# Performance work log

Hardware: AMD Instinct MI355X
Metric: run time of the kernel (lower is better)

## Reference

```python
import jax, jax.numpy as jnp
import numpy as np

B, C, H, W = 8, 768, 32, 32
NH = 12
HD = C // NH
HID = 4 * C
EPS = 1e-5


def _layer_norm(x, g, b):
    mu = jnp.mean(x, axis=-1, keepdims=True)
    var = jnp.mean(jnp.square(x - mu), axis=-1, keepdims=True)
    return (x - mu) * jax.lax.rsqrt(var + EPS) * g + b


def setup_inputs() -> dict:
    key = jax.random.key(0)
    ks = jax.random.split(key, 12)
    s = 0.02
    return {
        "x": jax.random.normal(ks[0], (B, C, H, W), jnp.float32),
        "conv_w": jax.random.normal(ks[1], (C, 1, 3, 3), jnp.float32) * s,  # depthwise OIHW
        "conv_b": jnp.zeros((C,), jnp.float32),
        "ln1_g": jnp.ones((C,), jnp.float32),
        "ln1_b": jnp.zeros((C,), jnp.float32),
        "qkv_w": jax.random.normal(ks[2], (3 * C, C), jnp.float32) * s,  # no bias (qkv_bias=False)
        "proj_w": jax.random.normal(ks[3], (C, C), jnp.float32) * s,
        "proj_b": jnp.zeros((C,), jnp.float32),
        "ln2_g": jnp.ones((C,), jnp.float32),
        "ln2_b": jnp.zeros((C,), jnp.float32),
        "fc1_w": jax.random.normal(ks[4], (HID, C), jnp.float32) * s,
        "fc1_b": jnp.zeros((HID,), jnp.float32),
        "fc2_w": jax.random.normal(ks[5], (C, HID), jnp.float32) * s,
        "fc2_b": jnp.zeros((C,), jnp.float32),
    }


def reference(x, conv_w, conv_b, ln1_g, ln1_b, qkv_w, proj_w, proj_b,
              ln2_g, ln2_b, fc1_w, fc1_b, fc2_w, fc2_b):
    # depthwise 3x3 conv positional embedding, residual
    pe = jax.lax.conv_general_dilated(
        x, conv_w, window_strides=(1, 1), padding=((1, 1), (1, 1)),
        dimension_numbers=("NCHW", "OIHW", "NCHW"), feature_group_count=C)
    x = x + pe + conv_b[None, :, None, None]

    b, c, h, w = x.shape
    t = x.reshape(b, c, h * w).transpose(0, 2, 1)  # [B, N, C]

    # attention
    hn = _layer_norm(t, ln1_g, ln1_b)
    qkv = hn @ qkv_w.T  # [B, N, 3C]
    qkv = qkv.reshape(b, h * w, 3, NH, HD).transpose(2, 0, 3, 1, 4)  # [3, B, nh, N, hd]
    q, k, v = qkv[0], qkv[1], qkv[2]
    scale = HD ** -0.5
    attn = jax.nn.softmax(jnp.einsum("bhnd,bhmd->bhnm", q, k) * scale, axis=-1)
    o = jnp.einsum("bhnm,bhmd->bhnd", attn, v).transpose(0, 2, 1, 3).reshape(b, h * w, c)
    t = t + (o @ proj_w.T + proj_b)

    # MLP
    hn = _layer_norm(t, ln2_g, ln2_b)
    hid = jax.nn.gelu(hn @ fc1_w.T + fc1_b, approximate=False)
    t = t + (hid @ fc2_w.T + fc2_b)

    return t.transpose(0, 2, 1).reshape(b, c, h, w)
```

## Files before the change

kernel.cpp:

```cpp
#include <hip/hip_runtime.h>
#include <math.h>


typedef __bf16 bf16;
typedef __attribute__((ext_vector_type(8))) __bf16 bf16x8;
typedef __attribute__((ext_vector_type(4))) __bf16 bf16x4;
typedef __attribute__((ext_vector_type(4))) float f32x4;

#define B_   8
#define C_   768
#define N_   1024
#define NH_  12
#define HD_  64
#define HID_ 3072
#define NTOK   (B_ * N_)
#define NHEADS (B_ * NH_)
#define FA_C   0.1803368801111601f

__device__ __forceinline__ void gload_lds16(const void* g, void* l) {
  __builtin_amdgcn_global_load_lds(
      (__attribute__((address_space(1))) void*)(void*)g,
      (__attribute__((address_space(3))) void*)l, 16, 0, 0);
}

__device__ __forceinline__ float gelu1(float x) {
  float u = 0.7978845608028654f * x * (1.0f + 0.044715f * x * x);
  float e = __builtin_amdgcn_exp2f(u * 2.885390081777927f);
  float th = 1.0f - 2.0f * __builtin_amdgcn_rcpf(e + 1.0f);
  return 0.5f * x * (1.0f + th);
}

#define PIPE_SYNC(N)                                              \
  do {                                                            \
    asm volatile("s_waitcnt vmcnt(" #N ") lgkmcnt(0)" ::: "memory"); \
    __builtin_amdgcn_sched_barrier(0);                            \
    __builtin_amdgcn_s_barrier();                                 \
    __builtin_amdgcn_sched_barrier(0);                            \
    asm volatile("" ::: "memory");                                \
  } while (0)

__global__ __launch_bounds__(512) void gemm_fc1(
    const bf16* __restrict__ A, const bf16* __restrict__ Bw,
    const float* __restrict__ bias, bf16* __restrict__ outp,
    int K, int lda, int ldb, int ntiles, int mtpx, int ldo) {
  __shared__ __align__(16) char smem[114688];
  const int tid = threadIdx.x;
  const int wave = tid >> 6, lane = tid & 63;
  const int wr = wave & 1, wc = wave >> 1;
  const int lr = lane & 15, kq = lane >> 4;

  const int bid = blockIdx.x;
  const int g = bid & 7, s = bid >> 3;
  const int ms = s / ntiles;
  const int m0 = (g * mtpx + ms) * 256;
  const int n0 = (s - ms * ntiles) * 192;

  f32x4 acc[8][3];
#pragma unroll
  for (int i = 0; i < 8; ++i)
#pragma unroll
    for (int j = 0; j < 3; ++j) acc[i][j] = (f32x4){0.f, 0.f, 0.f, 0.f};

  const bf16* pa[4];
  const bf16* pb[3];
  int da[4], db[3];
#pragma unroll
  for (int c = 0; c < 4; ++c) {
    const int sidx = c * 512 + tid;
    const int r = sidx >> 3, seg = (sidx & 7) ^ (r & 7);
    pa[c] = A + (size_t)(m0 + r) * lda + seg * 8;
    da[c] = sidx * 16;
  }
#pragma unroll
  for (int c = 0; c < 3; ++c) {
    const int sidx = c * 512 + tid;
    const int r = sidx >> 3, seg = (sidx & 7) ^ (r & 7);
    pb[c] = Bw + (size_t)(n0 + r) * ldb + seg * 8;
    db[c] = 32768 + sidx * 16;
  }

  const int NT = K >> 6;

  gload_lds16(pb[0], smem + db[0]);
  gload_lds16(pb[1], smem + db[1]);
  gload_lds16(pb[2], smem + db[2]);
  gload_lds16(pa[0], smem + da[0]);
  gload_lds16(pa[1], smem + da[1]);
  gload_lds16(pa[2], smem + da[2]);
  gload_lds16(pa[3], smem + da[3]);
#pragma unroll
  for (int c = 0; c < 4; ++c) pa[c] += 64;
#pragma unroll
  for (int c = 0; c < 3; ++c) pb[c] += 64;

  for (int t = 0; t < NT - 1; ++t) {
    const char* rb = smem + (t & 1) * 57344;
    char* wb = smem + ((t & 1) ^ 1) * 57344;
    bf16x8 af[4], bf0[3], bf1[3];

    PIPE_SYNC(1);
#pragma unroll
    for (int i = 0; i < 4; ++i) {
      const int r = wr * 128 + i * 16 + lr;
      af[i] = *(const bf16x8*)(rb + (r * 8 + (kq ^ (r & 7))) * 16);
    }
#pragma unroll
    for (int j = 0; j < 3; ++j) {
      const int r = wc * 48 + j * 16 + lr;
      bf0[j] = *(const bf16x8*)(rb + 32768 + (r * 8 + (kq ^ (r & 7))) * 16);
    }
    gload_lds16(pb[0], wb + db[0]); pb[0] += 64;
    gload_lds16(pb[1], wb + db[1]); pb[1] += 64;
    __builtin_amdgcn_s_setprio(1);
#pragma unroll
    for (int i = 0; i < 4; ++i)
#pragma unroll
      for (int j = 0; j < 3; ++j)
        acc[i][j] = __builtin_amdgcn_mfma_f32_16x16x32_bf16(bf0[j], af[i],
                                                            acc[i][j], 0, 0, 0);
    __builtin_amdgcn_s_setprio(0);

    PIPE_SYNC(2);
#pragma unroll
    for (int i = 0; i < 4; ++i) {
      const int r = wr * 128 + 64 + i * 16 + lr;
      af[i] = *(const bf16x8*)(rb + (r * 8 + (kq ^ (r & 7))) * 16);
    }
    gload_lds16(pb[2], wb + db[2]); pb[2] += 64;
    gload_lds16(pa[0], wb + da[0]); pa[0] += 64;
    __builtin_amdgcn_s_setprio(1);
#pragma unroll
    for (int i = 0; i < 4; ++i)
#pragma unroll
      for (int j = 0; j < 3; ++j)
        acc[4 + i][j] = __builtin_amdgcn_mfma_f32_16x16x32_bf16(
            bf0[j], af[i], acc[4 + i][j], 0, 0, 0);
    __builtin_amdgcn_s_setprio(0);

    PIPE_SYNC(4);
#pragma unroll
    for (int i = 0; i < 4; ++i) {
      const int r = wr * 128 + i * 16 + lr;
      af[i] = *(const bf16x8*)(rb + (r * 8 + ((4 + kq) ^ (r & 7))) * 16);
    }
#pragma unroll
    for (int j = 0; j < 3; ++j) {
      const int r = wc * 48 + j * 16 + lr;
      bf1[j] = *(const bf16x8*)(rb + 32768 + (r * 8 + ((4 + kq) ^ (r & 7))) * 16);
    }
    gload_lds16(pa[1], wb + da[1]); pa[1] += 64;
    gload_lds16(pa[2], wb + da[2]); pa[2] += 64;
    __builtin_amdgcn_s_setprio(1);
#pragma unroll
    for (int i = 0; i < 4; ++i)
#pragma unroll
      for (int j = 0; j < 3; ++j)
        acc[i][j] = __builtin_amdgcn_mfma_f32_16x16x32_bf16(bf1[j], af[i],
                                                            acc[i][j], 0, 0, 0);
    __builtin_amdgcn_s_setprio(0);

    PIPE_SYNC(6);
#pragma unroll
    for (int i = 0; i < 4; ++i) {
      const int r = wr * 128 + 64 + i * 16 + lr;
      af[i] = *(const bf16x8*)(rb + (r * 8 + ((4 + kq) ^ (r & 7))) * 16);
    }
    gload_lds16(pa[3], wb + da[3]); pa[3] += 64;
    __builtin_amdgcn_s_setprio(1);
#pragma unroll
    for (int i = 0; i < 4; ++i)
#pragma unroll
      for (int j = 0; j < 3; ++j)
        acc[4 + i][j] = __builtin_amdgcn_mfma_f32_16x16x32_bf16(
            bf1[j], af[i], acc[4 + i][j], 0, 0, 0);
    __builtin_amdgcn_s_setprio(0);
  }

  {
    const char* rb = smem + ((NT - 1) & 1) * 57344;
    bf16x8 af[4], bf0[3], bf1[3];
    PIPE_SYNC(0);
#pragma unroll
    for (int j = 0; j < 3; ++j) {
      const int r = wc * 48 + j * 16 + lr;
      bf0[j] = *(const bf16x8*)(rb + 32768 + (r * 8 + (kq ^ (r & 7))) * 16);
      bf1[j] = *(const bf16x8*)(rb + 32768 + (r * 8 + ((4 + kq) ^ (r & 7))) * 16);
    }
    __builtin_amdgcn_s_setprio(1);
#pragma unroll
    for (int half = 0; half < 2; ++half) {
#pragma unroll
      for (int i = 0; i < 4; ++i) {
        const int r = wr * 128 + half * 64 + i * 16 + lr;
        af[i] = *(const bf16x8*)(rb + (r * 8 + (kq ^ (r & 7))) * 16);
      }
#pragma unroll
      for (int i = 0; i < 4; ++i)
#pragma unroll
        for (int j = 0; j < 3; ++j)
          acc[half * 4 + i][j] = __builtin_amdgcn_mfma_f32_16x16x32_bf16(
              bf0[j], af[i], acc[half * 4 + i][j], 0, 0, 0);
#pragma unroll
      for (int i = 0; i < 4; ++i) {
        const int r = wr * 128 + half * 64 + i * 16 + lr;
        af[i] = *(const bf16x8*)(rb + (r * 8 + ((4 + kq) ^ (r & 7))) * 16);
      }
#pragma unroll
      for (int i = 0; i < 4; ++i)
#pragma unroll
        for (int j = 0; j < 3; ++j)
          acc[half * 4 + i][j] = __builtin_amdgcn_mfma_f32_16x16x32_bf16(
              bf1[j], af[i], acc[half * 4 + i][j], 0, 0, 0);
    }
    __builtin_amdgcn_s_setprio(0);
  }

#pragma unroll
  for (int j = 0; j < 3; ++j) {
    const int n = n0 + wc * 48 + j * 16 + kq * 4;
    const f32x4 bv = *(const f32x4*)(bias + n);
#pragma unroll
    for (int i = 0; i < 8; ++i) {
      const int m = m0 + wr * 128 + i * 16 + lr;
      const f32x4 v = acc[i][j];
      bf16x4 pk = {(bf16)gelu1(v[0] + bv[0]), (bf16)gelu1(v[1] + bv[1]),
                   (bf16)gelu1(v[2] + bv[2]), (bf16)gelu1(v[3] + bv[3])};
      *(bf16x4*)(outp + (size_t)m * ldo + n) = pk;
    }
  }
}

template <int BN, int EPI, bool REMAP>
__global__ __launch_bounds__(256) void gemm_bt(
    const bf16* __restrict__ A, const bf16* __restrict__ B, int K, int lda,
    int ldb, int ntiles, bf16* __restrict__ o0, bf16* __restrict__ o1,
    bf16* __restrict__ o2, float* __restrict__ resid,
    const float* __restrict__ bias, float* __restrict__ outp) {
  constexpr int JJ = BN / 32;
  constexpr int BCH = BN / 32;
  constexpr int STAGE_B = (128 + BN) * 64 * 2;
  constexpr int EXTRA_B = (EPI == 5) ? 64 * 132 * 4 : (EPI == 0 ? 128 * 256 : 0);
  constexpr int SMEM_B = STAGE_B > EXTRA_B ? STAGE_B : EXTRA_B;
  __shared__ __align__(16) char smemraw[SMEM_B];
  bf16* As = (bf16*)smemraw;
  bf16* Bs = As + 128 * 64;

  const int tid = threadIdx.x;
  const int wave = tid >> 6, lane = tid & 63;
  const int wm = wave & 1, wn = wave >> 1;
  const int lr = lane & 15, kq = lane >> 4;
  const int sw = lr & 7;

  int m0, n0;
  if constexpr (REMAP) {
    const int bid = blockIdx.x;
    const int g = bid & 7, s = bid >> 3;
    const int ms = s / ntiles;
    m0 = (g * 8 + ms) * 128;
    n0 = (s - ms * ntiles) * BN;
  } else {
    m0 = blockIdx.y * 128;
    n0 = blockIdx.x * BN;
  }

  f32x4 acc[4][JJ];
#pragma unroll
  for (int i = 0; i < 4; i++)
#pragma unroll
    for (int j = 0; j < JJ; j++) acc[i][j] = (f32x4){0.f, 0.f, 0.f, 0.f};

  const bf16* ap[4];
  const bf16* bp[BCH];
  {
    const bf16* Arow = A + (size_t)m0 * lda;
    const bf16* Brow = B + (size_t)n0 * ldb;
#pragma unroll
    for (int it = 0; it < 4; ++it) {
      int s = it * 256 + tid;
      int r = s >> 3, seg = (s & 7) ^ (r & 7);
      ap[it] = Arow + (size_t)r * lda + seg * 8;
    }
#pragma unroll
    for (int it = 0; it < BCH; ++it) {
      int s = it * 256 + tid;
      int r = s >> 3, seg = (s & 7) ^ (r & 7);
      bp[it] = Brow + (size_t)r * ldb + seg * 8;
    }
  }

  for (int k0 = 0; k0 < K; k0 += 64) {
#pragma unroll
    for (int it = 0; it < 4; ++it) {
      gload_lds16(ap[it], (char*)As + (it * 256 + tid) * 16);
      ap[it] += 64;
    }
#pragma unroll
    for (int it = 0; it < BCH; ++it) {
      gload_lds16(bp[it], (char*)Bs + (it * 256 + tid) * 16);
      bp[it] += 64;
    }
    __syncthreads();

#pragma unroll
    for (int h = 0; h < 2; ++h) {
      bf16x8 af[4], bfr[JJ];
      const int c = h * 4 + kq;
#pragma unroll
      for (int i = 0; i < 4; i++) {
        int row = wm * 64 + i * 16 + lr;
        af[i] = *(const bf16x8*)((char*)As + (row * 8 + (c ^ sw)) * 16);
      }
#pragma unroll
      for (int j = 0; j < JJ; j++) {
        int row = wn * (BN / 2) + j * 16 + lr;
        bfr[j] = *(const bf16x8*)((char*)Bs + (row * 8 + (c ^ sw)) * 16);
      }
#pragma unroll
      for (int i = 0; i < 4; i++)
#pragma unroll
        for (int j = 0; j < JJ; j++)
          acc[i][j] = __builtin_amdgcn_mfma_f32_16x16x32_bf16(bfr[j], af[i],
                                                              acc[i][j], 0, 0, 0);
    }
    __syncthreads();
  }

  if constexpr (EPI == 0) {
    const int b = m0 >> 10, tok0 = m0 & (N_ - 1);
    if (n0 < 2 * C_) {
      const int s = n0 >= C_ ? 1 : 0;
      bf16* dst = s ? o1 : o0;
#pragma unroll
      for (int i = 0; i < 4; i++) {
        const int m = m0 + wm * 64 + i * 16 + lr;
#pragma unroll
        for (int j = 0; j < JJ; j++) {
          const int rem = n0 - s * C_ + wn * (BN / 2) + j * 16 + kq * 4;
          const int h = rem >> 6, d = rem & 63;
          const f32x4 v = acc[i][j];
          bf16x4 pk = {(bf16)v[0], (bf16)v[1], (bf16)v[2], (bf16)v[3]};
          size_t head = (size_t)b * NH_ + h;
          *(bf16x4*)(dst + (head * N_ + (m & (N_ - 1))) * HD_ + d) = pk;
        }
      }
    } else {
      bf16* tile = (bf16*)smemraw;
#pragma unroll
      for (int i = 0; i < 4; i++) {
        const int ml = wm * 64 + i * 16 + lr;
        const int mc = ml >> 3, mo = ml & 7;
#pragma unroll
        for (int j = 0; j < JJ; j++) {
          const f32x4 v = acc[i][j];
#pragma unroll
          for (int r = 0; r < 4; r++) {
            const int nl = wn * (BN / 2) + j * 16 + kq * 4 + r;
            *(bf16*)((char*)tile + nl * 256 + ((mc ^ (nl & 15)) * 16) + mo * 2) =
                (bf16)v[r];
          }
        }
      }
      __syncthreads();
      const int nl = tid >> 1, mh = (tid & 1) * 64;
      const int vb = n0 - 2 * C_ + nl;
      const size_t head = (size_t)b * NH_ + (vb >> 6);
      bf16* dst = o2 + (head * HD_ + (vb & 63)) * N_ + tok0 + mh;
#pragma unroll
      for (int c8 = 0; c8 < 8; ++c8) {
        const int c = (mh >> 3) + c8;
        bf16x8 val = *(const bf16x8*)((char*)tile + nl * 256 +
                                      ((c ^ (nl & 15)) * 16));
        *(bf16x8*)(dst + c8 * 8) = val;
      }
    }
  } else if constexpr (EPI == 3) {
#pragma unroll
    for (int j = 0; j < JJ; j++) {
      const int n = n0 + wn * (BN / 2) + j * 16 + kq * 4;
      const f32x4 bv = *(const f32x4*)(bias + n);
#pragma unroll
      for (int i = 0; i < 4; i++) {
        const int m = m0 + wm * 64 + i * 16 + lr;
        float* rp = resid + (size_t)m * C_ + n;
        f32x4 old = *(const f32x4*)rp;
        const f32x4 v = acc[i][j];
        f32x4 nw = {old[0] + v[0] + bv[0], old[1] + v[1] + bv[1],
                    old[2] + v[2] + bv[2], old[3] + v[3] + bv[3]};
        *(f32x4*)rp = nw;
      }
    }
  } else if constexpr (EPI == 5) {
    float* tile = (float*)smemraw;
    const int b = m0 >> 10, tok0 = m0 & (N_ - 1);
#pragma unroll
    for (int j = 0; j < JJ; j++) {
      const int nl0 = wn * (BN / 2) + j * 16 + kq * 4;
      const int n = n0 + nl0;
      const f32x4 bv = *(const f32x4*)(bias + n);
#pragma unroll
      for (int i = 0; i < 4; i++) {
        const int ml = wm * 64 + i * 16 + lr;
        const float* rp = resid + (size_t)(m0 + ml) * C_ + n;
        f32x4 old = *(const f32x4*)rp;
        const f32x4 v = acc[i][j];
#pragma unroll
        for (int r = 0; r < 4; r++)
          tile[(nl0 + r) * 132 + ml] = old[r] + v[r] + bv[r];
      }
    }
    __syncthreads();
    const int nl = tid & 63, mc = tid >> 6;
    float* dst = outp + ((size_t)(b * C_ + n0 + nl)) * N_ + tok0 + mc * 32;
    const float* src = tile + nl * 132 + mc * 32;
#pragma unroll
    for (int q = 0; q < 8; ++q)
      *(f32x4*)(dst + q * 4) = *(const f32x4*)(src + q * 4);
  }
}

__global__ __launch_bounds__(256, 3) void flash_attn(
    const bf16* __restrict__ Qb, const bf16* __restrict__ Kb,
    const bf16* __restrict__ Vt, bf16* __restrict__ attn) {
  __shared__ __align__(16) bf16 ksm[2][64 * 64];
  __shared__ __align__(16) bf16 vsm[2][64 * 64];
  __shared__ __align__(16) bf16 psm[4][32 * 64];

  const int tid = threadIdx.x, wave = tid >> 6, lane = tid & 63;
  const int lr = lane & 15, kq = lane >> 4;
  const int head = blockIdx.y;
  const int b = head / NH_, hh = head - b * NH_;
  const int q0 = blockIdx.x * 128;
  const bf16* Qh = Qb + (size_t)head * (N_ * HD_);
  const bf16* Kh = Kb + (size_t)head * (N_ * HD_);
  const bf16* Vh = Vt + (size_t)head * (HD_ * N_);
  char* pw = (char*)&psm[wave][0];

  bf16x8 qf[2][2];
#pragma unroll
  for (int j = 0; j < 2; ++j)
#pragma unroll
    for (int kh = 0; kh < 2; ++kh)
      qf[j][kh] = *(const bf16x8*)(Qh +
                                   (size_t)(q0 + wave * 32 + j * 16 + lr) * HD_ +
                                   kh * 32 + kq * 8);

  f32x4 o[4][2];
#pragma unroll
  for (int i = 0; i < 4; i++)
#pragma unroll
    for (int j = 0; j < 2; j++) o[i][j] = (f32x4){0.f, 0.f, 0.f, 0.f};
  float mprev[2] = {-1e30f, -1e30f}, lacc[2] = {0.f, 0.f};

  auto stage = [&](int t, int bi) {
#pragma unroll
    for (int it = 0; it < 2; ++it) {
      int s = it * 256 + tid;
      int r = s >> 3, seg = (s & 7) ^ (r & 7);
      gload_lds16(Kh + (size_t)(t * 64 + r) * HD_ + seg * 8,
                  (char*)ksm[bi] + (it * 256 + wave * 64) * 16);
    }
#pragma unroll
    for (int it = 0; it < 2; ++it) {
      int s = it * 256 + tid;
      int r = s >> 3, seg = (s & 7) ^ (r & 7);
      gload_lds16(Vh + (size_t)r * N_ + t * 64 + seg * 8,
                  (char*)vsm[bi] + (it * 256 + wave * 64) * 16);
    }
  };

  stage(0, 0);

  for (int t = 0; t < 16; ++t) {
    const int bi = t & 1;
    __syncthreads();
    if (t < 15) stage(t + 1, bi ^ 1);

    f32x4 sacc[4][2];
#pragma unroll
    for (int i = 0; i < 4; ++i) {
#pragma unroll
      for (int j = 0; j < 2; ++j) sacc[i][j] = (f32x4){0.f, 0.f, 0.f, 0.f};
      int row = i * 16 + lr;
      bf16x8 kf0 = *(const bf16x8*)((char*)ksm[bi] + row * 128 +
                                    ((kq ^ (row & 7)) * 16));
      bf16x8 kf1 = *(const bf16x8*)((char*)ksm[bi] + row * 128 +
                                    (((4 + kq) ^ (row & 7)) * 16));
#pragma unroll
      for (int j = 0; j < 2; ++j) {
        sacc[i][j] = __builtin_amdgcn_mfma_f32_16x16x32_bf16(kf0, qf[j][0],
                                                             sacc[i][j], 0, 0, 0);
        sacc[i][j] = __builtin_amdgcn_mfma_f32_16x16x32_bf16(kf1, qf[j][1],
                                                             sacc[i][j], 0, 0, 0);
      }
    }

#pragma unroll
    for (int j = 0; j < 2; ++j) {
      float mx = -1e30f;
#pragma unroll
      for (int i = 0; i < 4; ++i)
#pragma unroll
        for (int r = 0; r < 4; ++r) mx = fmaxf(mx, sacc[i][j][r]);
      mx = fmaxf(mx, __shfl_xor(mx, 16));
      mx = fmaxf(mx, __shfl_xor(mx, 32));
      float mnew = fmaxf(mprev[j], mx);
      float alpha = __builtin_amdgcn_exp2f((mprev[j] - mnew) * FA_C);
      mprev[j] = mnew;
      float rs = 0.f;
      const int prow = j * 16 + lr;
#pragma unroll
      for (int i = 0; i < 4; ++i) {
        float p0 = __builtin_amdgcn_exp2f((sacc[i][j][0] - mnew) * FA_C);
        float p1 = __builtin_amdgcn_exp2f((sacc[i][j][1] - mnew) * FA_C);
        float p2 = __builtin_amdgcn_exp2f((sacc[i][j][2] - mnew) * FA_C);
        float p3 = __builtin_amdgcn_exp2f((sacc[i][j][3] - mnew) * FA_C);
        rs += (p0 + p1) + (p2 + p3);
        bf16x4 pk = {(bf16)p0, (bf16)p1, (bf16)p2, (bf16)p3};
        int c = i * 2 + (kq >> 1);
        *(bf16x4*)(pw + prow * 128 + ((c ^ (prow & 7)) * 16) + (kq & 1) * 8) = pk;
      }
      rs += __shfl_xor(rs, 16);
      rs += __shfl_xor(rs, 32);
      lacc[j] = lacc[j] * alpha + rs;
#pragma unroll
      for (int i = 0; i < 4; ++i) {
        o[i][j][0] *= alpha; o[i][j][1] *= alpha;
        o[i][j][2] *= alpha; o[i][j][3] *= alpha;
      }
    }

#pragma unroll
    for (int k0c = 0; k0c < 2; ++k0c) {
      bf16x8 pf[2];
#pragma unroll
      for (int j = 0; j < 2; ++j) {
        int prow = j * 16 + lr, c = k0c * 4 + kq;
        pf[j] = *(const bf16x8*)(pw + prow * 128 + ((c ^ (prow & 7)) * 16));
      }
#pragma unroll
      for (int i = 0; i < 4; ++i) {
        int d = i * 16 + lr, c = k0c * 4 + kq;
        bf16x8 vf = *(const bf16x8*)((char*)vsm[bi] + d * 128 +
                                     ((c ^ (d & 7)) * 16));
#pragma unroll
        for (int j = 0; j < 2; ++j)
          o[i][j] = __builtin_amdgcn_mfma_f32_16x16x32_bf16(vf, pf[j], o[i][j],
                                                            0, 0, 0);
      }
    }
  }

#pragma unroll
  for (int j = 0; j < 2; ++j) {
    float inv = 1.0f / lacc[j];
    int tok = q0 + wave * 32 + j * 16 + lr;
    bf16* op = attn + ((size_t)(b * N_ + tok)) * C_ + hh * HD_;
#pragma unroll
    for (int i = 0; i < 4; ++i) {
      bf16x4 pk = {(bf16)(o[i][j][0] * inv), (bf16)(o[i][j][1] * inv),
                   (bf16)(o[i][j][2] * inv), (bf16)(o[i][j][3] * inv)};
      *(bf16x4*)(op + i * 16 + kq * 4) = pk;
    }
  }
}

__global__ __launch_bounds__(256) void cast_all(
    const float* __restrict__ a, int na, const float* __restrict__ b, int nb,
    const float* __restrict__ c, int nc, const float* __restrict__ d,
    bf16* __restrict__ dst) {
  int i = (blockIdx.x * 256 + threadIdx.x) * 4;
  const float* src;
  int off;
  if (i < na) { src = a; off = i; }
  else if (i < na + nb) { src = b; off = i - na; }
  else if (i < na + nb + nc) { src = c; off = i - na - nb; }
  else { src = d; off = i - na - nb - nc; }
  float4 v = *(const float4*)(src + off);
  bf16x4 o = {(bf16)v.x, (bf16)v.y, (bf16)v.z, (bf16)v.w};
  *(bf16x4*)(dst + i) = o;
}

__global__ __launch_bounds__(256) void conv_pe_t(const float* __restrict__ x,
                                                 const float* __restrict__ cw,
                                                 const float* __restrict__ cb,
                                                 float* __restrict__ t0) {
  __shared__ float tile[32][33];
  const int h = blockIdx.x, ct = blockIdx.y, b = blockIdx.z;
  const int tid = threadIdx.x;
  const int w = tid & 31, cs = tid >> 5;
#pragma unroll
  for (int cc = cs; cc < 32; cc += 8) {
    int c = ct * 32 + cc;
    const float* xp = x + ((size_t)(b * C_ + c)) * 1024;
    const float* wp = cw + c * 9;
    float s = cb[c] + xp[h * 32 + w];
#pragma unroll
    for (int ky = 0; ky < 3; ++ky) {
      int hy = h + ky - 1;
      if ((unsigned)hy < 32u) {
#pragma unroll
        for (int kx = 0; kx < 3; ++kx) {
          int wx = w + kx - 1;
          if ((unsigned)wx < 32u) s += xp[hy * 32 + wx] * wp[ky * 3 + kx];
        }
      }
    }
    tile[cc][w] = s;
  }
  __syncthreads();
  const int cc = tid & 31;
#pragma unroll
  for (int wc = tid >> 5; wc < 32; wc += 8)
    t0[((size_t)(b * N_) + h * 32 + wc) * C_ + ct * 32 + cc] = tile[cc][wc];
}

__global__ __launch_bounds__(256) void ln_bf16(const float* __restrict__ t,
                                               const float* __restrict__ g,
                                               const float* __restrict__ be,
                                               bf16* __restrict__ out) {
  int row = blockIdx.x, tid = threadIdx.x;
  const float* p = t + (size_t)row * C_;
  float v0 = p[tid], v1 = p[tid + 256], v2 = p[tid + 512];
  __shared__ float rs[256], rq[256];
  rs[tid] = v0 + v1 + v2;
  rq[tid] = v0 * v0 + v1 * v1 + v2 * v2;
  __syncthreads();
  for (int off = 128; off; off >>= 1) {
    if (tid < off) {
      rs[tid] += rs[tid + off];
      rq[tid] += rq[tid + off];
    }
    __syncthreads();
  }
  float mu = rs[0] * (1.f / C_);
  float var = rq[0] * (1.f / C_) - mu * mu;
  float rstd = rsqrtf(var + 1e-5f);
  bf16* q = out + (size_t)row * C_;
  q[tid] = (bf16)((v0 - mu) * rstd * g[tid] + be[tid]);
  q[tid + 256] = (bf16)((v1 - mu) * rstd * g[tid + 256] + be[tid + 256]);
  q[tid + 512] = (bf16)((v2 - mu) * rstd * g[tid + 512] + be[tid + 512]);
}

extern "C" void kernel_launch(void* const* d_in, const int* in_sizes, int n_in,
                              void* d_out, int out_size, void* d_ws,
                              size_t ws_size, hipStream_t stream) {
  (void)in_sizes; (void)n_in; (void)out_size; (void)ws_size;
  const float* x      = (const float*)d_in[0];
  const float* conv_w = (const float*)d_in[1];
  const float* conv_b = (const float*)d_in[2];
  const float* ln1_g  = (const float*)d_in[3];
  const float* ln1_b  = (const float*)d_in[4];
  const float* qkv_w  = (const float*)d_in[5];
  const float* proj_w = (const float*)d_in[6];
  const float* proj_b = (const float*)d_in[7];
  const float* ln2_g  = (const float*)d_in[8];
  const float* ln2_b  = (const float*)d_in[9];
  const float* fc1_w  = (const float*)d_in[10];
  const float* fc1_b  = (const float*)d_in[11];
  const float* fc2_w  = (const float*)d_in[12];
  const float* fc2_b  = (const float*)d_in[13];
  float* out = (float*)d_out;

  char* w = (char*)d_ws;
  auto carve = [&](size_t bytes) {
    char* p = w;
    w += (bytes + 255) & ~(size_t)255;
    return p;
  };
  bf16* hid   = (bf16*)carve((size_t)NTOK * HID_ * 2);
  float* t0   = (float*)carve((size_t)NTOK * C_ * 4);
  bf16* lnout = (bf16*)carve((size_t)NTOK * C_ * 2);
  bf16* wq    = (bf16*)carve((size_t)3 * C_ * C_ * 2);
  bf16* wp    = (bf16*)carve((size_t)C_ * C_ * 2);
  bf16* w1    = (bf16*)carve((size_t)HID_ * C_ * 2);
  bf16* w2    = (bf16*)carve((size_t)C_ * HID_ * 2);
  bf16* Qb    = (bf16*)carve((size_t)NHEADS * N_ * HD_ * 2);
  bf16* Kb    = (bf16*)carve((size_t)NHEADS * N_ * HD_ * 2);
  bf16* Vt    = (bf16*)carve((size_t)NHEADS * HD_ * N_ * 2);
  bf16* attn  = (bf16*)carve((size_t)NTOK * C_ * 2);

  const int na = 3 * C_ * C_, nb = C_ * C_, nc = HID_ * C_, nd = C_ * HID_;
  cast_all<<<(na + nb + nc + nd) / 1024, 256, 0, stream>>>(
      qkv_w, na, proj_w, nb, fc1_w, nc, fc2_w, wq);

  conv_pe_t<<<dim3(32, C_ / 32, B_), 256, 0, stream>>>(x, conv_w, conv_b, t0);

  ln_bf16<<<NTOK, 256, 0, stream>>>(t0, ln1_g, ln1_b, lnout);
  gemm_bt<128, 0, true><<<1152, 256, 0, stream>>>(
      lnout, wq, 768, 768, 768, 18, Qb, Kb, Vt, nullptr, nullptr, nullptr);

  flash_attn<<<dim3(N_ / 128, NHEADS), 256, 0, stream>>>(Qb, Kb, Vt, attn);

  gemm_bt<64, 3, true><<<768, 256, 0, stream>>>(
      attn, wp, 768, 768, 768, 12, nullptr, nullptr, nullptr, t0, proj_b,
      nullptr);
  ln_bf16<<<NTOK, 256, 0, stream>>>(t0, ln2_g, ln2_b, lnout);
  gemm_fc1<<<512, 512, 0, stream>>>(lnout, w1, fc1_b, hid, 768, 768, 768,
                                    16, 4, HID_);
  gemm_bt<64, 5, true><<<768, 256, 0, stream>>>(
      hid, w2, 3072, 3072, 3072, 12, nullptr, nullptr, nullptr, t0, fc2_b,
      out);
}
```

Measured before the change: 385.7 us.

## Add dedicated 512-thread triple-buffered FC2 GEMM with larger N tile

Replaces the generic gemm_bt<64,5> FC2 kernel with a dedicated 512-thread kernel. It uses 128x192 tiles, a three-stage global-to-LDS pipeline with direct LDS loads, and a sliced transposed residual epilogue. The larger tiles are meant to raise data reuse and cut redundant A loads over K=3072, and the deeper pipeline hides memory latency. The launch drops to 256 blocks, which may leave some CUs underused, and the large LDS footprint limits occupancy to one block per CU.

New measurement: 395.2 us. +2.5%, slower.

```diff
diff --git a/kernel.cpp b/kernel.cpp
--- a/kernel.cpp
+++ b/kernel.cpp
@@ -39,6 +39,176 @@
     asm volatile("" ::: "memory");                                \
   } while (0)
 
+__global__ __launch_bounds__(512) void gemm_fc2(
+    const bf16* __restrict__ A, const bf16* __restrict__ Bw,
+    const float* __restrict__ bias, const float* __restrict__ resid,
+    float* __restrict__ outp, int K, int lda, int ldb) {
+  __shared__ __align__(16) char smem[122880];
+  const int tid = threadIdx.x;
+  const int wave = tid >> 6, lane = tid & 63;
+  const int wr = wave & 1, wc = wave >> 1;
+  const int lr = lane & 15, kq = lane >> 4;
+
+  const int bid = blockIdx.x;
+  const int g = bid & 7, s = bid >> 3;
+  const int ms = s >> 2;
+  const int m0 = (g * 8 + ms) * 128;
+  const int n0 = (s & 3) * 192;
+
+  f32x4 acc[4][3];
+#pragma unroll
+  for (int i = 0; i < 4; ++i)
+#pragma unroll
+    for (int j = 0; j < 3; ++j) acc[i][j] = (f32x4){0.f, 0.f, 0.f, 0.f};
+
+  const bf16* pa[2];
+  const bf16* pb[3];
+  int da[2], db[3];
+#pragma unroll
+  for (int c = 0; c < 2; ++c) {
+    const int sidx = c * 512 + tid;
+    const int r = sidx >> 3, seg = (sidx & 7) ^ (r & 7);
+    pa[c] = A + (size_t)(m0 + r) * lda + seg * 8;
+    da[c] = sidx * 16;
+  }
+#pragma unroll
+  for (int c = 0; c < 3; ++c) {
+    const int sidx = c * 512 + tid;
+    const int r = sidx >> 3, seg = (sidx & 7) ^ (r & 7);
+    pb[c] = Bw + (size_t)(n0 + r) * ldb + seg * 8;
+    db[c] = 16384 + sidx * 16;
+  }
+
+  const int NT = K >> 6;
+
+#pragma unroll
+  for (int tt = 0; tt < 2; ++tt) {
+    char* wb = smem + tt * 40960;
+    gload_lds16(pb[0], wb + db[0]);
+    gload_lds16(pb[1], wb + db[1]);
+    gload_lds16(pb[2], wb + db[2]);
+    gload_lds16(pa[0], wb + da[0]);
+    gload_lds16(pa[1], wb + da[1]);
+    pb[0] += 64; pb[1] += 64; pb[2] += 64; pa[0] += 64; pa[1] += 64;
+  }
+
+  int cur = 0;
+  for (int t = 0; t < NT - 1; ++t) {
+    const char* rb = smem + cur * 40960;
+    PIPE_SYNC(5);
+    if (t < NT - 2) {
+      int wi = cur + 2; if (wi >= 3) wi -= 3;
+      char* wb = smem + wi * 40960;
+      gload_lds16(pb[0], wb + db[0]); pb[0] += 64;
+      gload_lds16(pb[1], wb + db[1]); pb[1] += 64;
+      gload_lds16(pb[2], wb + db[2]); pb[2] += 64;
+      gload_lds16(pa[0], wb + da[0]); pa[0] += 64;
+      gload_lds16(pa[1], wb + da[1]); pa[1] += 64;
+    }
+    bf16x8 af[4], bf[3];
+#pragma unroll
+    for (int i = 0; i < 4; ++i) {
+      const int r = wr * 64 + i * 16 + lr;
+      af[i] = *(const bf16x8*)(rb + (r * 8 + (kq ^ (r & 7))) * 16);
+    }
+#pragma unroll
+    for (int j = 0; j < 3; ++j) {
+      const int r = wc * 48 + j * 16 + lr;
+      bf[j] = *(const bf16x8*)(rb + 16384 + (r * 8 + (kq ^ (r & 7))) * 16);
+    }
+    __builtin_amdgcn_s_setprio(1);
+#pragma unroll
+    for (int i = 0; i < 4; ++i)
+#pragma unroll
+      for (int j = 0; j < 3; ++j)
+        acc[i][j] = __builtin_amdgcn_mfma_f32_16x16x32_bf16(bf[j], af[i],
+                                                            acc[i][j], 0, 0, 0);
+    __builtin_amdgcn_s_setprio(0);
+#pragma unroll
+    for (int i = 0; i < 4; ++i) {
+      const int r = wr * 64 + i * 16 + lr;
+      af[i] = *(const bf16x8*)(rb + (r * 8 + ((4 + kq) ^ (r & 7))) * 16);
+    }
+#pragma unroll
+    for (int j = 0; j < 3; ++j) {
+      const int r = wc * 48 + j * 16 + lr;
+      bf[j] = *(const bf16x8*)(rb + 16384 + (r * 8 + ((4 + kq) ^ (r & 7))) * 16);
+    }
+    __builtin_amdgcn_s_setprio(1);
+#pragma unroll
+    for (int i = 0; i < 4; ++i)
+#pragma unroll
+      for (int j = 0; j < 3; ++j)
+        acc[i][j] = __builtin_amdgcn_mfma_f32_16x16x32_bf16(bf[j], af[i],
+                                                            acc[i][j], 0, 0, 0);
+    __builtin_amdgcn_s_setprio(0);
+    if (++cur == 3) cur = 0;
+  }
+
+  {
+    const char* rb = smem + cur * 40960;
+    bf16x8 af[4], bf[3];
+    PIPE_SYNC(0);
+#pragma unroll
+    for (int kh = 0; kh < 2; ++kh) {
+      const int c0 = kh * 4 + kq;
+#pragma unroll
+      for (int i = 0; i < 4; ++i) {
+        const int r = wr * 64 + i * 16 + lr;
+        af[i] = *(const bf16x8*)(rb + (r * 8 + (c0 ^ (r & 7))) * 16);
+      }
+#pragma unroll
+      for (int j = 0; j < 3; ++j) {
+        const int r = wc * 48 + j * 16 + lr;
+        bf[j] = *(const bf16x8*)(rb + 16384 + (r * 8 + (c0 ^ (r & 7))) * 16);
+      }
+      __builtin_amdgcn_s_setprio(1);
+#pragma unroll
+      for (int i = 0; i < 4; ++i)
+#pragma unroll
+        for (int j = 0; j < 3; ++j)
+          acc[i][j] = __builtin_amdgcn_mfma_f32_16x16x32_bf16(bf[j], af[i],
+                                                              acc[i][j], 0, 0, 0);
+      __builtin_amdgcn_s_setprio(0);
+    }
+  }
+
+  {
+    float* tile = (float*)smem;
+    const int b = m0 >> 10, tok0 = m0 & (N_ - 1);
+#pragma unroll
+    for (int sl = 0; sl < 3; ++sl) {
+      __syncthreads();
+#pragma unroll
+      for (int j = 0; j < 3; ++j) {
+        const int nl0 = wc * 48 + j * 16 + kq * 4;
+        if (((wc * 48 + j * 16) >> 6) == sl) {
+          const int n = n0 + nl0;
+          const f32x4 bv = *(const f32x4*)(bias + n);
+#pragma unroll
+          for (int i = 0; i < 4; ++i) {
+            const int ml = wr * 64 + i * 16 + lr;
+            const float* rp = resid + (size_t)(m0 + ml) * C_ + n;
+            f32x4 old = *(const f32x4*)rp;
+            const f32x4 v = acc[i][j];
+#pragma unroll
+            for (int r = 0; r < 4; ++r)
+              tile[(nl0 - sl * 64 + r) * 132 + ml] = old[r] + v[r] + bv[r];
+          }
+        }
+      }
+      __syncthreads();
+      const int nl = tid & 63, mc = tid >> 6;
+      float* dst = outp + ((size_t)(b * C_ + n0 + sl * 64 + nl)) * N_ +
+                   tok0 + mc * 16;
+      const float* src = tile + nl * 132 + mc * 16;
+#pragma unroll
+      for (int q = 0; q < 4; ++q)
+        *(f32x4*)(dst + q * 4) = *(const f32x4*)(src + q * 4);
+    }
+  }
+}
+
 __global__ __launch_bounds__(512) void gemm_fc1(
     const bf16* __restrict__ A, const bf16* __restrict__ Bw,
     const float* __restrict__ bias, bf16* __restrict__ outp,
@@ -239,7 +409,7 @@
   constexpr int JJ = BN / 32;
   constexpr int BCH = BN / 32;
   constexpr int STAGE_B = (128 + BN) * 64 * 2;
-  constexpr int EXTRA_B = (EPI == 5) ? 64 * 132 * 4 : (EPI == 0 ? 128 * 256 : 0);
+  constexpr int EXTRA_B = (EPI == 0 ? 128 * 256 : 0);
   constexpr int SMEM_B = STAGE_B > EXTRA_B ? STAGE_B : EXTRA_B;
   __shared__ __align__(16) char smemraw[SMEM_B];
   bf16* As = (bf16*)smemraw;
@@ -389,32 +559,6 @@
         *(f32x4*)rp = nw;
       }
     }
-  } else if constexpr (EPI == 5) {
-    float* tile = (float*)smemraw;
-    const int b = m0 >> 10, tok0 = m0 & (N_ - 1);
-#pragma unroll
-    for (int j = 0; j < JJ; j++) {
-      const int nl0 = wn * (BN / 2) + j * 16 + kq * 4;
-      const int n = n0 + nl0;
-      const f32x4 bv = *(const f32x4*)(bias + n);
-#pragma unroll
-      for (int i = 0; i < 4; i++) {
-        const int ml = wm * 64 + i * 16 + lr;
-        const float* rp = resid + (size_t)(m0 + ml) * C_ + n;
-        f32x4 old = *(const f32x4*)rp;
-        const f32x4 v = acc[i][j];
-#pragma unroll
-        for (int r = 0; r < 4; r++)
-          tile[(nl0 + r) * 132 + ml] = old[r] + v[r] + bv[r];
-      }
-    }
-    __syncthreads();
-    const int nl = tid & 63, mc = tid >> 6;
-    float* dst = outp + ((size_t)(b * C_ + n0 + nl)) * N_ + tok0 + mc * 32;
-    const float* src = tile + nl * 132 + mc * 32;
-#pragma unroll
-    for (int q = 0; q < 8; ++q)
-      *(f32x4*)(dst + q * 4) = *(const f32x4*)(src + q * 4);
   }
 }
 
@@ -697,7 +841,5 @@
   ln_bf16<<<NTOK, 256, 0, stream>>>(t0, ln2_g, ln2_b, lnout);
   gemm_fc1<<<512, 512, 0, stream>>>(lnout, w1, fc1_b, hid, 768, 768, 768,
                                     16, 4, HID_);
-  gemm_bt<64, 5, true><<<768, 256, 0, stream>>>(
-      hid, w2, 3072, 3072, 3072, 12, nullptr, nullptr, nullptr, t0, fc2_b,
-      out);
-}
+  gemm_fc2<<<256, 512, 0, stream>>>(hid, w2, fc2_b, t0, out, 3072, 3072, 3072);
+}
```
